# Performance work log

Measured on AMD Instinct MI355X. Metric: run time of the kernel, lower is better.

Reference implementation:

```python
import jax, jax.numpy as jnp
import numpy as np

BS, N, D, H = 4, 2048, 512, 8
DK = D // H
XAVIER_STD = float(np.sqrt(2.0 / (D + D)))  # xavier_normal_, gain=1


def setup_inputs() -> dict:
    key = jax.random.key(0)
    ks = jax.random.split(key, 10)
    Q = jax.random.normal(ks[0], (BS, N, D), jnp.float32)
    K = jax.random.normal(ks[1], (BS, N, D), jnp.float32)
    V = jax.random.normal(ks[2], (BS, N, D), jnp.float32)
    q_mas = jax.random.randint(ks[3], (BS, N, 1), 0, 2).astype(jnp.float32)
    k_mas = jax.random.randint(ks[4], (BS, N, 1), 0, 2).astype(jnp.float32)
    # 0/1 attention mask; force self-edges so no row is fully masked (avoids NaN softmax)
    att_mas = jax.random.randint(ks[5], (BS, N, N), 0, 2).astype(jnp.float32)
    att_mas = jnp.maximum(att_mas, jnp.eye(N, dtype=jnp.float32)[None])
    WQ = jax.random.normal(ks[6], (D, D), jnp.float32) * XAVIER_STD
    WK = jax.random.normal(ks[7], (D, D), jnp.float32) * XAVIER_STD
    WV = jax.random.normal(ks[8], (D, D), jnp.float32) * XAVIER_STD
    WO = jax.random.normal(ks[9], (D, D), jnp.float32) * XAVIER_STD
    return {"Q": Q, "K": K, "V": V, "q_mas": q_mas, "k_mas": k_mas,
            "att_mas": att_mas, "WQ": WQ, "WK": WK, "WV": WV, "WO": WO}


def reference(Q, K, V, q_mas, k_mas, att_mas, WQ, WK, WV, WO):
    bs, n, d = Q.shape
    h, dk = H, DK
    qm = q_mas.reshape(bs, 1, n, 1)  # (bs,1,n,1)
    km = k_mas.reshape(bs, 1, n, 1)
    # nn.Linear (no bias): x @ W.T ; split heads -> (bs,h,n,dk); apply pre-masks
    Qh = qm * (Q @ WQ.T).reshape(bs, n, h, dk).transpose(0, 2, 1, 3)
    Kh = km * (K @ WK.T).reshape(bs, n, h, dk).transpose(0, 2, 1, 3)
    Vh = km * (V @ WV.T).reshape(bs, n, h, dk).transpose(0, 2, 1, 3)
    scores = jnp.einsum('bhqd,bhkd->bhqk', Qh, Kh) / jnp.sqrt(jnp.float32(dk))
    mas = att_mas.reshape(bs, 1, n, n)
    scores = jnp.where(mas.astype(bool), scores, -jnp.inf)
    attn = jax.nn.softmax(scores, axis=-1) * mas
    y = jnp.einsum('bhqk,bhkd->bhqd', attn, Vh) * km  # post-mask (note: km over query dim, as in source)
    y = y.transpose(0, 2, 1, 3).reshape(bs, n, d)
    y = (y @ WO.T) * k_mas.reshape(bs, n, 1)
    return y
```

## Files before the change

kernel.cpp:

```cpp
#include <hip/hip_runtime.h>


#define BS_    4
#define NSEQ   2048
#define DMODEL 512
#define NH     8
#define DKH    64
#define MROWS  (BS_ * NSEQ)
#define NW32   (NSEQ / 32)
#define NWORDS (BS_ * NSEQ * NSEQ / 32)

typedef unsigned short ushort_t;
typedef __attribute__((ext_vector_type(8))) short short8;
typedef __attribute__((ext_vector_type(4))) float floatx4;

__device__ __forceinline__ ushort_t f2bf(float f) {
    unsigned int x = __builtin_bit_cast(unsigned int, f);
    unsigned int lsb = (x >> 16) & 1u;
    x += 0x7fffu + lsb;
    return (ushort_t)(x >> 16);
}
__device__ __forceinline__ floatx4 mfma_bf16(short8 a, short8 b, floatx4 c) {
    return __builtin_amdgcn_mfma_f32_16x16x32_bf16(a, b, c, 0, 0, 0);
}
__device__ __forceinline__ void gld16(const ushort_t* g, ushort_t* l) {
    __builtin_amdgcn_global_load_lds(
        (const __attribute__((address_space(1))) unsigned int*)g,
        (__attribute__((address_space(3))) unsigned int*)l, 16, 0, 0);
}
__device__ __forceinline__ unsigned int cvt_pk_bf16(float lo, float hi) {
    unsigned int r;
    asm("v_cvt_pk_bf16_f32 %0, %1, %2" : "=v"(r) : "v"(lo), "v"(hi));
    return r;
}
__device__ __forceinline__ float fexp2(float x) {
#if __has_builtin(__builtin_amdgcn_exp2f)
    return __builtin_amdgcn_exp2f(x);
#else
    return exp2f(x);
#endif
}
__device__ __forceinline__ void permlane32_swap(unsigned& a, unsigned& b) {
    asm volatile("v_permlane32_swap_b32 %0, %1" : "+v"(a), "+v"(b));
}
__device__ __forceinline__ void permlane16_swap(unsigned& a, unsigned& b) {
    asm volatile("v_permlane16_swap_b32 %0, %1" : "+v"(a), "+v"(b));
}
__device__ __forceinline__ unsigned spread4(unsigned b) {
    b = (b | (b << 12)) & 0x000F000Fu;
    b = (b | (b << 6))  & 0x03030303u;
    b = (b | (b << 3))  & 0x11111111u;
    return b;
}

__global__ __launch_bounds__(256) void cvt_all(const float* __restrict__ a,
                                               const float* __restrict__ b,
                                               const float* __restrict__ c,
                                               const float* __restrict__ wq,
                                               const float* __restrict__ wk,
                                               const float* __restrict__ wv,
                                               const float* __restrict__ wo,
                                               const float* __restrict__ am,
                                               ushort_t* __restrict__ dst,
                                               ushort_t* __restrict__ wdst,
                                               unsigned int* __restrict__ mb, int n4) {
    const int i = blockIdx.x * blockDim.x + threadIdx.x;
    const int yy = blockIdx.y;
    if (yy >= 4) {
        const int g = ((yy - 4) * 4096 + blockIdx.x) * 256 + threadIdx.x;
        const float4 v = ((const float4*)am)[g];
        const unsigned long long b0 = __ballot(v.x != 0.f);
        const unsigned long long b1 = __ballot(v.y != 0.f);
        const unsigned long long b2 = __ballot(v.z != 0.f);
        const unsigned long long b3 = __ballot(v.w != 0.f);
        const int l = threadIdx.x & 63;
        if (l < 8) {
            const unsigned B0 = (unsigned)((b0 >> (8 * l)) & 0xFFull);
            const unsigned B1 = (unsigned)((b1 >> (8 * l)) & 0xFFull);
            const unsigned B2 = (unsigned)((b2 >> (8 * l)) & 0xFFull);
            const unsigned B3 = (unsigned)((b3 >> (8 * l)) & 0xFFull);
            const unsigned w = spread4(B0) | (spread4(B1) << 1) |
                               (spread4(B2) << 2) | (spread4(B3) << 3);
            const int g0 = g & ~63;
            mb[(g0 >> 3) + l] = w;
        }
        return;
    }
    if (yy == 3) {
        const int wn4 = DMODEL * DMODEL / 4;
        if (i < 4 * wn4) {
            const int w = i >> 16;
            const float* src = (w == 0) ? wq : (w == 1) ? wk : (w == 2) ? wv : wo;
            const float4 v = ((const float4*)src)[i & (wn4 - 1)];
            ushort4 o;
            o.x = f2bf(v.x); o.y = f2bf(v.y); o.z = f2bf(v.z); o.w = f2bf(v.w);
            ((ushort4*)wdst)[i] = o;
        }
        return;
    }
    const float* src = (yy == 0) ? a : (yy == 1) ? b : c;
    ushort_t* d = dst + (size_t)yy * ((size_t)n4 * 4);
    const float4 v = ((const float4*)src)[i];
    ushort4 o;
    o.x = f2bf(v.x); o.y = f2bf(v.y); o.z = f2bf(v.z); o.w = f2bf(v.w);
    ((ushort4*)d)[i] = o;
}

__global__ __launch_bounds__(256) void gemm_proj(const ushort_t* __restrict__ Xall,
                                                 const ushort_t* __restrict__ Wall,
                                                 const float* __restrict__ qmas,
                                                 const float* __restrict__ kmas,
                                                 ushort_t* __restrict__ Qh,
                                                 ushort_t* __restrict__ Kh,
                                                 ushort_t* __restrict__ Vt) {
    __shared__ ushort_t As[64 * 64];
    __shared__ ushort_t Bs[64 * 64];
    const int z = blockIdx.z;
    const ushort_t* X  = Xall + (size_t)z * MROWS * DMODEL;
    const ushort_t* Wb = Wall + (size_t)z * DMODEL * DMODEL;
    const float* rowmask = (z == 0) ? qmas : kmas;

    const int tid  = threadIdx.x;
    const int wave = tid >> 6;
    const int lane = tid & 63;
    const int l16  = lane & 15;
    const int quad = lane >> 4;
    const int wr   = wave >> 1;
    const int wc   = wave & 1;
    const int m0   = blockIdx.x * 64;
    const int n0   = blockIdx.y * 64;

    floatx4 acc[2][2];
#pragma unroll
    for (int t = 0; t < 2; ++t)
#pragma unroll
        for (int u = 0; u < 2; ++u) acc[t][u] = (floatx4){0.f, 0.f, 0.f, 0.f};

    for (int k0 = 0; k0 < DMODEL; k0 += 64) {
#pragma unroll
        for (int i = 0; i < 2; ++i) {
            const int cch = tid + i * 256;
            const int row = cch >> 3;
            const int sc  = 8 * ((cch & 7) ^ (row & 7));
            gld16(X  + (size_t)(m0 + row) * DMODEL + k0 + sc, &As[cch * 8]);
            gld16(Wb + (size_t)(n0 + row) * DMODEL + k0 + sc, &Bs[cch * 8]);
        }
        __syncthreads();
#pragma unroll
        for (int kk = 0; kk < 64; kk += 32) {
            const int pc = (((kk >> 3) | quad) ^ (l16 & 7)) * 8;
            short8 a[2], b[2];
#pragma unroll
            for (int t = 0; t < 2; ++t)
                a[t] = *(const short8*)&As[(wr * 32 + t * 16 + l16) * 64 + pc];
#pragma unroll
            for (int u = 0; u < 2; ++u)
                b[u] = *(const short8*)&Bs[(wc * 32 + u * 16 + l16) * 64 + pc];
#pragma unroll
            for (int t = 0; t < 2; ++t)
#pragma unroll
                for (int u = 0; u < 2; ++u) acc[t][u] = mfma_bf16(a[t], b[u], acc[t][u]);
        }
        __syncthreads();
    }

    float rm[2][4];
#pragma unroll
    for (int t = 0; t < 2; ++t)
#pragma unroll
        for (int r = 0; r < 4; ++r)
            rm[t][r] = rowmask[m0 + wr * 32 + t * 16 + quad * 4 + r];
    if (z == 0) {
#pragma unroll
        for (int t = 0; t < 2; ++t)
#pragma unroll
            for (int r = 0; r < 4; ++r) rm[t][r] *= 0.18033688011112042f;
    }

    const int bb    = m0 >> 11;
    const int nbase = (m0 & (NSEQ - 1)) + wr * 32;
#pragma unroll
    for (int t = 0; t < 2; ++t) {
#pragma unroll
        for (int u = 0; u < 2; ++u) {
            const int d = n0 + wc * 32 + u * 16 + l16;
            const int h = d >> 6, cc = d & 63;
            if (z < 2) {
                ushort_t* dst = (z == 0) ? Qh : Kh;
#pragma unroll
                for (int r = 0; r < 4; ++r) {
                    const int n = nbase + t * 16 + quad * 4 + r;
                    dst[((size_t)(bb * NH + h) * NSEQ + n) * DKH + cc] =
                        f2bf(acc[t][u][r] * rm[t][r]);
                }
            } else {
                ushort4 pk;
                pk.x = f2bf(acc[t][u][0] * rm[t][0]);
                pk.y = f2bf(acc[t][u][1] * rm[t][1]);
                pk.z = f2bf(acc[t][u][2] * rm[t][2]);
                pk.w = f2bf(acc[t][u][3] * rm[t][3]);
                const int n = nbase + t * 16 + quad * 4;
                *(ushort4*)(Vt + ((size_t)(bb * NH + h) * DKH + cc) * NSEQ + n) = pk;
            }
        }
    }
}

__global__ __launch_bounds__(256) void gemm_out(const ushort_t* __restrict__ X,
                                                const ushort_t* __restrict__ Wb,
                                                const float* __restrict__ rowmask,
                                                float* __restrict__ dst) {
    __shared__ ushort_t As[64 * 64];
    __shared__ ushort_t Bs[64 * 64];
    const int tid  = threadIdx.x;
    const int wave = tid >> 6;
    const int lane = tid & 63;
    const int l16  = lane & 15;
    const int quad = lane >> 4;
    const int wr   = wave >> 1;
    const int wc   = wave & 1;
    const int m0   = blockIdx.x * 64;
    const int n0   = blockIdx.y * 64;

    floatx4 acc[2][2];
#pragma unroll
    for (int t = 0; t < 2; ++t)
#pragma unroll
        for (int u = 0; u < 2; ++u) acc[t][u] = (floatx4){0.f, 0.f, 0.f, 0.f};

    for (int k0 = 0; k0 < DMODEL; k0 += 64) {
#pragma unroll
        for (int i = 0; i < 2; ++i) {
            const int cch = tid + i * 256;
            const int row = cch >> 3;
            const int sc  = 8 * ((cch & 7) ^ (row & 7));
            gld16(X  + (size_t)(m0 + row) * DMODEL + k0 + sc, &As[cch * 8]);
            gld16(Wb + (size_t)(n0 + row) * DMODEL + k0 + sc, &Bs[cch * 8]);
        }
        __syncthreads();
#pragma unroll
        for (int kk = 0; kk < 64; kk += 32) {
            const int pc = (((kk >> 3) | quad) ^ (l16 & 7)) * 8;
            short8 a[2], b[2];
#pragma unroll
            for (int t = 0; t < 2; ++t)
                a[t] = *(const short8*)&As[(wr * 32 + t * 16 + l16) * 64 + pc];
#pragma unroll
            for (int u = 0; u < 2; ++u)
                b[u] = *(const short8*)&Bs[(wc * 32 + u * 16 + l16) * 64 + pc];
#pragma unroll
            for (int t = 0; t < 2; ++t)
#pragma unroll
                for (int u = 0; u < 2; ++u) acc[t][u] = mfma_bf16(a[t], b[u], acc[t][u]);
        }
        __syncthreads();
    }

#pragma unroll
    for (int t = 0; t < 2; ++t) {
#pragma unroll
        for (int r = 0; r < 4; ++r) {
            const int m = m0 + wr * 32 + t * 16 + quad * 4 + r;
            const float rm = rowmask[m];
#pragma unroll
            for (int u = 0; u < 2; ++u) {
                const int d = n0 + wc * 32 + u * 16 + l16;
                dst[(size_t)m * DMODEL + d] = acc[t][u][r] * rm;
            }
        }
    }
}

__global__ __launch_bounds__(256) void attn_kernel(const ushort_t* __restrict__ Qh,
                                                   const ushort_t* __restrict__ Kh,
                                                   const ushort_t* __restrict__ Vt,
                                                   const unsigned int* __restrict__ Mb,
                                                   const float* __restrict__ kmas,
                                                   ushort_t* __restrict__ y) {
    __shared__ __align__(16) ushort_t Ks[128 * 72];
    __shared__ __align__(16) ushort_t Vs[64 * 136];

    const int tid  = threadIdx.x;
    const int lane = tid & 63;
    const int wave = tid >> 6;
    const int l16  = lane & 15;
    const int quad = lane >> 4;
    const int h    = blockIdx.y;
    const int b    = blockIdx.z;
    const int qw   = blockIdx.x * 128 + wave * 32;

    const ushort_t* Kb = Kh + (size_t)(b * NH + h) * NSEQ * DKH;
    const ushort_t* Vb = Vt + (size_t)(b * NH + h) * DKH * NSEQ;
    const uint4* Mv0 = (const uint4*)(Mb + ((size_t)(b * NSEQ + qw) + l16) * NW32);
    const uint4* Mv1 = (const uint4*)(Mb + ((size_t)(b * NSEQ + qw) + 16 + l16) * NW32);

    const ushort_t* Qp0 = Qh + ((size_t)((b * NH + h) * NSEQ) + qw + l16) * DKH + quad * 8;
    const ushort_t* Qp1 = Qp0 + 16 * DKH;
    const short8 qf0a = *(const short8*)Qp0;
    const short8 qf0b = *(const short8*)(Qp0 + 32);
    const short8 qf1a = *(const short8*)Qp1;
    const short8 qf1b = *(const short8*)(Qp1 + 32);

    const short8 ones = {(short)0x3F80, (short)0x3F80, (short)0x3F80, (short)0x3F80,
                         (short)0x3F80, (short)0x3F80, (short)0x3F80, (short)0x3F80};

    floatx4 accA[4], accB[4];
    floatx4 accL0 = (floatx4){0.f, 0.f, 0.f, 0.f};
    floatx4 accL1 = (floatx4){0.f, 0.f, 0.f, 0.f};
#pragma unroll
    for (int ct = 0; ct < 4; ++ct) {
        accA[ct] = (floatx4){0.f, 0.f, 0.f, 0.f};
        accB[ct] = (floatx4){0.f, 0.f, 0.f, 0.f};
    }

#define SFRAG(FR, PX0, PY0, PX1, PY1) do {                                         \
    const short8 ka = *(const short8*)&Ks[((FR) * 16 + l16) * 72 + quad * 8];      \
    const short8 kb = *(const short8*)&Ks[((FR) * 16 + l16) * 72 + 32 + quad * 8]; \
    floatx4 s0 = {0.f, 0.f, 0.f, 0.f};                                             \
    s0 = mfma_bf16(ka, qf0a, s0);                                                  \
    s0 = mfma_bf16(kb, qf0b, s0);                                                  \
    floatx4 s1 = {0.f, 0.f, 0.f, 0.f};                                             \
    s1 = mfma_bf16(ka, qf1a, s1);                                                  \
    s1 = mfma_bf16(kb, qf1b, s1);                                                  \
    float p0[4], p1[4];                                                            \
    _Pragma("unroll")                                                              \
    for (int r = 0; r < 4; ++r) {                                                  \
        const int bitp = (((FR) & 1) << 4) + r;                                    \
        const unsigned m0m =                                                       \
            (unsigned)__builtin_amdgcn_sbfe((int)wsh0[(FR) >> 1], bitp, 1);        \
        const unsigned m1m =                                                       \
            (unsigned)__builtin_amdgcn_sbfe((int)wsh1[(FR) >> 1], bitp, 1);        \
        p0[r] = __builtin_bit_cast(float,                                          \
                    __builtin_bit_cast(unsigned, fexp2(s0[r])) & m0m);             \
        p1[r] = __builtin_bit_cast(float,                                          \
                    __builtin_bit_cast(unsigned, fexp2(s1[r])) & m1m);             \
    }                                                                              \
    PX0 = cvt_pk_bf16(p0[0], p0[1]); PY0 = cvt_pk_bf16(p0[2], p0[3]);              \
    PX1 = cvt_pk_bf16(p1[0], p1[1]); PY1 = cvt_pk_bf16(p1[2], p1[3]);              \
} while (0)

    for (int kt = 0; kt < NSEQ / 128; ++kt) {
        const int k0 = kt * 128;

        short8 kv[4], vv[4];
#pragma unroll
        for (int i = 0; i < 4; ++i) {
            const int c = tid + i * 256;
            kv[i] = *(const short8*)(Kb + (size_t)(k0 + (c >> 3)) * DKH + (c & 7) * 8);
        }
#pragma unroll
        for (int i = 0; i < 4; ++i) {
            const int c = tid + i * 256;
            vv[i] = *(const short8*)(Vb + (size_t)(c >> 4) * NSEQ + k0 + (c & 15) * 8);
        }
        const uint4 mw0 = Mv0[kt];
        const uint4 mw1 = Mv1[kt];

        __syncthreads();
#pragma unroll
        for (int i = 0; i < 4; ++i) {
            const int c = tid + i * 256;
            *(short8*)&Ks[(c >> 3) * 72 + (c & 7) * 8] = kv[i];
        }
#pragma unroll
        for (int i = 0; i < 4; ++i) {
            const int c = tid + i * 256;
            *(short8*)&Vs[(c >> 4) * 136 + (c & 15) * 8] = vv[i];
        }
        __syncthreads();

        const unsigned int wsh0[4] = {mw0.x >> (quad * 4), mw0.y >> (quad * 4),
                                      mw0.z >> (quad * 4), mw0.w >> (quad * 4)};
        const unsigned int wsh1[4] = {mw1.x >> (quad * 4), mw1.y >> (quad * 4),
                                      mw1.z >> (quad * 4), mw1.w >> (quad * 4)};

#pragma unroll
        for (int kf = 0; kf < 4; ++kf) {
            unsigned xe0, ye0, xo0, yo0;
            unsigned xe1, ye1, xo1, yo1;
            SFRAG(kf * 2,     xe0, ye0, xe1, ye1);
            SFRAG(kf * 2 + 1, xo0, yo0, xo1, yo1);

            permlane32_swap(xe0, xo0); permlane32_swap(ye0, yo0);
            permlane16_swap(xe0, xo0); permlane16_swap(ye0, yo0);
            permlane32_swap(xe1, xo1); permlane32_swap(ye1, yo1);
            permlane16_swap(xe1, xo1); permlane16_swap(ye1, yo1);

            const uint4 u0 = {xe0, ye0, xo0, yo0};
            const uint4 u1 = {xe1, ye1, xo1, yo1};
            const short8 pf0 = __builtin_bit_cast(short8, u0);
            const short8 pf1 = __builtin_bit_cast(short8, u1);

            accL0 = mfma_bf16(pf0, ones, accL0);
            accL1 = mfma_bf16(pf1, ones, accL1);

#pragma unroll
            for (int ct = 0; ct < 4; ++ct) {
                const short8 vb =
                    *(const short8*)&Vs[(ct * 16 + l16) * 136 + kf * 32 + quad * 8];
                accA[ct] = mfma_bf16(pf0, vb, accA[ct]);
                accB[ct] = mfma_bf16(pf1, vb, accB[ct]);
            }
        }
    }
#undef SFRAG

#pragma unroll
    for (int r = 0; r < 4; ++r) {
        const int q0 = qw + quad * 4 + r;
        const int q1 = q0 + 16;
        const float sc0 = kmas[b * NSEQ + q0] / accL0[r];
        const float sc1 = kmas[b * NSEQ + q1] / accL1[r];
#pragma unroll
        for (int ct = 0; ct < 4; ++ct) {
            y[(size_t)(b * NSEQ + q0) * DMODEL + h * DKH + ct * 16 + l16] =
                f2bf(accA[ct][r] * sc0);
            y[(size_t)(b * NSEQ + q1) * DMODEL + h * DKH + ct * 16 + l16] =
                f2bf(accB[ct][r] * sc1);
        }
    }
}

extern "C" void kernel_launch(void* const* d_in, const int* in_sizes, int n_in,
                              void* d_out, int out_size, void* d_ws, size_t ws_size,
                              hipStream_t stream) {
    (void)in_sizes; (void)n_in; (void)out_size; (void)ws_size;
    const float* Q  = (const float*)d_in[0];
    const float* K  = (const float*)d_in[1];
    const float* V  = (const float*)d_in[2];
    const float* qm = (const float*)d_in[3];
    const float* km = (const float*)d_in[4];
    const float* am = (const float*)d_in[5];
    const float* WQ = (const float*)d_in[6];
    const float* WK = (const float*)d_in[7];
    const float* WV = (const float*)d_in[8];
    const float* WO = (const float*)d_in[9];

    const size_t XN = (size_t)MROWS * DMODEL;
    const size_t WN = (size_t)DMODEL * DMODEL;
    ushort_t* Xbf = (ushort_t*)d_ws;
    ushort_t* Wbf = Xbf + 3 * XN;
    ushort_t* WOb = Wbf + 3 * WN;
    ushort_t* Qh  = Wbf + 4 * WN;
    ushort_t* Kh  = Qh + XN;
    ushort_t* Vt  = Kh + XN;
    ushort_t* y   = Vt + XN;
    unsigned int* Mbits = (unsigned int*)d_out;
    float* out = (float*)d_out;

    hipLaunchKernelGGL(cvt_all, dim3(4096, 8), dim3(256), 0, stream,
                       Q, K, V, WQ, WK, WV, WO, am, Xbf, Wbf, Mbits, (int)(XN / 4));

    hipLaunchKernelGGL(gemm_proj, dim3(MROWS / 64, DMODEL / 64, 3), dim3(256), 0, stream,
                       Xbf, Wbf, qm, km, Qh, Kh, Vt);

    hipLaunchKernelGGL(attn_kernel, dim3(NSEQ / 128, NH, BS_), dim3(256), 0, stream,
                       Qh, Kh, Vt, Mbits, km, y);

    hipLaunchKernelGGL(gemm_out, dim3(MROWS / 64, DMODEL / 64), dim3(256), 0, stream,
                       y, WOb, km, out);
}
```

Measured before the change: 243.8 us.

## Double-buffer K/V shared tiles and prefetch next tile during compute

```diff
diff --git a/kernel.cpp b/kernel.cpp
--- a/kernel.cpp
+++ b/kernel.cpp
@@ -271,14 +271,14 @@
     }
 }
 
-__global__ __launch_bounds__(256) void attn_kernel(const ushort_t* __restrict__ Qh,
-                                                   const ushort_t* __restrict__ Kh,
-                                                   const ushort_t* __restrict__ Vt,
-                                                   const unsigned int* __restrict__ Mb,
-                                                   const float* __restrict__ kmas,
-                                                   ushort_t* __restrict__ y) {
-    __shared__ __align__(16) ushort_t Ks[128 * 72];
-    __shared__ __align__(16) ushort_t Vs[64 * 136];
+__global__ __launch_bounds__(256, 2) void attn_kernel(const ushort_t* __restrict__ Qh,
+                                                      const ushort_t* __restrict__ Kh,
+                                                      const ushort_t* __restrict__ Vt,
+                                                      const unsigned int* __restrict__ Mb,
+                                                      const float* __restrict__ kmas,
+                                                      ushort_t* __restrict__ y) {
+    __shared__ __align__(16) ushort_t Ks[2][128 * 72];
+    __shared__ __align__(16) ushort_t Vs[2][64 * 136];
 
     const int tid  = threadIdx.x;
     const int lane = tid & 63;
@@ -313,61 +313,81 @@
         accB[ct] = (floatx4){0.f, 0.f, 0.f, 0.f};
     }
 
-#define SFRAG(FR, PX0, PY0, PX1, PY1) do {                                         \
-    const short8 ka = *(const short8*)&Ks[((FR) * 16 + l16) * 72 + quad * 8];      \
-    const short8 kb = *(const short8*)&Ks[((FR) * 16 + l16) * 72 + 32 + quad * 8]; \
-    floatx4 s0 = {0.f, 0.f, 0.f, 0.f};                                             \
-    s0 = mfma_bf16(ka, qf0a, s0);                                                  \
-    s0 = mfma_bf16(kb, qf0b, s0);                                                  \
-    floatx4 s1 = {0.f, 0.f, 0.f, 0.f};                                             \
-    s1 = mfma_bf16(ka, qf1a, s1);                                                  \
-    s1 = mfma_bf16(kb, qf1b, s1);                                                  \
-    float p0[4], p1[4];                                                            \
-    _Pragma("unroll")                                                              \
-    for (int r = 0; r < 4; ++r) {                                                  \
-        const int bitp = (((FR) & 1) << 4) + r;                                    \
-        const unsigned m0m =                                                       \
-            (unsigned)__builtin_amdgcn_sbfe((int)wsh0[(FR) >> 1], bitp, 1);        \
-        const unsigned m1m =                                                       \
-            (unsigned)__builtin_amdgcn_sbfe((int)wsh1[(FR) >> 1], bitp, 1);        \
-        p0[r] = __builtin_bit_cast(float,                                          \
-                    __builtin_bit_cast(unsigned, fexp2(s0[r])) & m0m);             \
-        p1[r] = __builtin_bit_cast(float,                                          \
-                    __builtin_bit_cast(unsigned, fexp2(s1[r])) & m1m);             \
-    }                                                                              \
-    PX0 = cvt_pk_bf16(p0[0], p0[1]); PY0 = cvt_pk_bf16(p0[2], p0[3]);              \
-    PX1 = cvt_pk_bf16(p1[0], p1[1]); PY1 = cvt_pk_bf16(p1[2], p1[3]);              \
+#define SFRAG(FR, PX0, PY0, PX1, PY1) do {                                          \
+    const short8 ka = *(const short8*)&Ksb[((FR) * 16 + l16) * 72 + quad * 8];      \
+    const short8 kb = *(const short8*)&Ksb[((FR) * 16 + l16) * 72 + 32 + quad * 8]; \
+    floatx4 s0 = {0.f, 0.f, 0.f, 0.f};                                              \
+    s0 = mfma_bf16(ka, qf0a, s0);                                                   \
+    s0 = mfma_bf16(kb, qf0b, s0);                                                   \
+    floatx4 s1 = {0.f, 0.f, 0.f, 0.f};                                              \
+    s1 = mfma_bf16(ka, qf1a, s1);                                                   \
+    s1 = mfma_bf16(kb, qf1b, s1);                                                   \
+    float p0[4], p1[4];                                                             \
+    _Pragma("unroll")                                                               \
+    for (int r = 0; r < 4; ++r) {                                                   \
+        const int bitp = (((FR) & 1) << 4) + r;                                     \
+        const unsigned m0m =                                                        \
+            (unsigned)__builtin_amdgcn_sbfe((int)wsh0[(FR) >> 1], bitp, 1);         \
+        const unsigned m1m =                                                        \
+            (unsigned)__builtin_amdgcn_sbfe((int)wsh1[(FR) >> 1], bitp, 1);         \
+        p0[r] = __builtin_bit_cast(float,                                           \
+                    __builtin_bit_cast(unsigned, fexp2(s0[r])) & m0m);              \
+        p1[r] = __builtin_bit_cast(float,                                           \
+                    __builtin_bit_cast(unsigned, fexp2(s1[r])) & m1m);              \
+    }                                                                               \
+    PX0 = cvt_pk_bf16(p0[0], p0[1]); PY0 = cvt_pk_bf16(p0[2], p0[3]);               \
+    PX1 = cvt_pk_bf16(p1[0], p1[1]); PY1 = cvt_pk_bf16(p1[2], p1[3]);               \
 } while (0)
 
+    short8 kv[4], vv[4];
+    uint4 mw0n, mw1n;
+#pragma unroll
+    for (int i = 0; i < 4; ++i) {
+        const int c = tid + i * 256;
+        kv[i] = *(const short8*)(Kb + (size_t)(c >> 3) * DKH + (c & 7) * 8);
+    }
+#pragma unroll
+    for (int i = 0; i < 4; ++i) {
+        const int c = tid + i * 256;
+        vv[i] = *(const short8*)(Vb + (size_t)(c >> 4) * NSEQ + (c & 15) * 8);
+    }
+    mw0n = Mv0[0];
+    mw1n = Mv1[0];
+
     for (int kt = 0; kt < NSEQ / 128; ++kt) {
-        const int k0 = kt * 128;
-
-        short8 kv[4], vv[4];
+        ushort_t* Ksb = Ks[kt & 1];
+        ushort_t* Vsb = Vs[kt & 1];
+
 #pragma unroll
         for (int i = 0; i < 4; ++i) {
             const int c = tid + i * 256;
-            kv[i] = *(const short8*)(Kb + (size_t)(k0 + (c >> 3)) * DKH + (c & 7) * 8);
+            *(short8*)&Ksb[(c >> 3) * 72 + (c & 7) * 8] = kv[i];
         }
 #pragma unroll
         for (int i = 0; i < 4; ++i) {
             const int c = tid + i * 256;
-            vv[i] = *(const short8*)(Vb + (size_t)(c >> 4) * NSEQ + k0 + (c & 15) * 8);
-        }
-        const uint4 mw0 = Mv0[kt];
-        const uint4 mw1 = Mv1[kt];
+            *(short8*)&Vsb[(c >> 4) * 136 + (c & 15) * 8] = vv[i];
+        }
+        const uint4 mw0 = mw0n;
+        const uint4 mw1 = mw1n;
 
         __syncthreads();
-#pragma unroll
-        for (int i = 0; i < 4; ++i) {
-            const int c = tid + i * 256;
-            *(short8*)&Ks[(c >> 3) * 72 + (c & 7) * 8] = kv[i];
-        }
-#pragma unroll
-        for (int i = 0; i < 4; ++i) {
-            const int c = tid + i * 256;
-            *(short8*)&Vs[(c >> 4) * 136 + (c & 15) * 8] = vv[i];
-        }
-        __syncthreads();
+
+        if (kt + 1 < NSEQ / 128) {
+            const int kn = (kt + 1) * 128;
+#pragma unroll
+            for (int i = 0; i < 4; ++i) {
+                const int c = tid + i * 256;
+                kv[i] = *(const short8*)(Kb + (size_t)(kn + (c >> 3)) * DKH + (c & 7) * 8);
+            }
+#pragma unroll
+            for (int i = 0; i < 4; ++i) {
+                const int c = tid + i * 256;
+                vv[i] = *(const short8*)(Vb + (size_t)(c >> 4) * NSEQ + kn + (c & 15) * 8);
+            }
+            mw0n = Mv0[kt + 1];
+            mw1n = Mv1[kt + 1];
+        }
 
         const unsigned int wsh0[4] = {mw0.x >> (quad * 4), mw0.y >> (quad * 4),
                                       mw0.z >> (quad * 4), mw0.w >> (quad * 4)};
@@ -397,7 +417,7 @@
 #pragma unroll
             for (int ct = 0; ct < 4; ++ct) {
                 const short8 vb =
-                    *(const short8*)&Vs[(ct * 16 + l16) * 136 + kf * 32 + quad * 8];
+                    *(const short8*)&Vsb[(ct * 16 + l16) * 136 + kf * 32 + quad * 8];
                 accA[ct] = mfma_bf16(pf0, vb, accA[ct]);
                 accB[ct] = mfma_bf16(pf1, vb, accB[ct]);
             }
```

Result: no change. 243.2 us (-0.2%).
